# Performance work log

Measured on AMD Instinct MI355X. Metric: run time of the kernel, lower is better.

Reference implementation:

```python
import math
import jax, jax.numpy as jnp
import numpy as np
from jax import lax

L = 16
T = 256
FDIM = 3
N_MIN = 4
N_MAX = 64
INIT_RANGE = 1e-4
# low 32 bits of the products are exact in uint32, and XOR + (% T) with T=256
# only reads the low 8 bits, so uint32 arithmetic matches torch's int64 exactly.
PI = jnp.array([1, 2654435761, 805459861], dtype=jnp.uint32)

def _levels():
    growth = math.exp(math.log(N_MAX / N_MIN) / (L - 1))
    return [math.floor(N_MIN * growth ** l) for l in range(L)]

def setup_inputs() -> dict:
    key = jax.random.key(0)
    kx, kt = jax.random.split(key)
    x = jax.random.uniform(kx, (4, 3, 64, 64, 64), dtype=jnp.float32)
    hash_table = (jax.random.uniform(kt, (L, T, FDIM), dtype=jnp.float32) * 2.0
                  - 1.0) * INIT_RANGE
    return {"x": x, "hash_table": hash_table}

def _forward(x, hash_table):
    b, c, h, w, d = x.shape
    outs = []
    for l, n in enumerate(_levels()):
        kh, kw, kd = h // n, w // n, d // n
        # max_pool3d with kernel==stride, VALID padding (torch default)
        pooled = lax.reduce_window(x * n, -jnp.inf, lax.max,
                                   (1, 1, kh, kw, kd), (1, 1, kh, kw, kd),
                                   'VALID')  # [b, 3, nh, nw, nd]
        g = pooled.astype(jnp.uint32)  # trunc toward zero (values >= 0)
        g = g * PI.reshape(1, 3, 1, 1, 1)
        gh = (g[:, 0] ^ g[:, 1] ^ g[:, 2]) % jnp.uint32(T)  # [b, nh, nw, nd]
        feat = hash_table[l][gh]                 # [b, nh, nw, nd, F] gather
        feat = jnp.transpose(feat, (0, 4, 1, 3, 2))  # [b, F, nh, nd, nw]
        up = jax.image.resize(feat, (b, FDIM, h, w, d), method='trilinear')
        outs.append(up)
    return jnp.concatenate(outs, axis=1)  # [b, L*F, h, w, d]

def reference(x, hash_table):
    return _forward(x, hash_table)
```

## Files before the change

### kernel.cpp

```cpp
#include <hip/hip_runtime.h>
#include <cmath>
#include <cstdint>
#include <cstddef>

using u32 = unsigned int;
typedef float f32x4 __attribute__((ext_vector_type(4)));

__device__ inline void nt_store4(float* p, float a, float b, float c, float d)
{
    f32x4 v; v.x = a; v.y = b; v.z = c; v.w = d;
    __builtin_nontemporal_store(v, (f32x4*)p);
}

constexpr int NH[12] = {4,4,5,6,8,10,12,16,21,21,32,32};

constexpr int OFF_M2  = 0;
constexpr int OFF_M3  = 393216;
constexpr int OFF_M5  = 504348;
constexpr int OFF_M4  = 525084;
constexpr int OFF_M6  = 574236;
constexpr int OFF_M8  = 586236;
constexpr int OFF_M10 = 592380;
constexpr int OFF_M12 = 594972;
constexpr int OFF_M16 = 596472;

constexpr int GOFF[12] = {149310,149566,149822,150322,151186,153234,
                          157234,164146,180530,217574,254618,385690};

constexpr float invf_of(int nh){ return (float)(1.0/(64.0/(double)nh)); }
constexpr float INVF[12] = {invf_of(4),invf_of(4),invf_of(5),invf_of(6),
                            invf_of(8),invf_of(10),invf_of(12),invf_of(16),
                            invf_of(21),invf_of(21),invf_of(32),invf_of(32)};

struct HP { int n[16]; };

__device__ inline float lp(float a, float b, float w){ return fmaf(w, b - a, a); }

__device__ inline void hash_store(const float* __restrict__ tbl, float4* __restrict__ g4,
                                  int goff, int lvl, int n,
                                  float m0, float m1, float m2, int idx)
{
    float nf = (float)n;
    u32 g0 = (u32)(m0 * nf);
    u32 g1 = ((u32)(m1 * nf)) * 2654435761u;
    u32 g2 = ((u32)(m2 * nf)) * 805459861u;
    u32 h  = (g0 ^ g1 ^ g2) & 255u;
    const float* te = tbl + ((size_t)lvl * 256 + h) * 3;
    g4[goff + idx] = make_float4(te[0], te[1], te[2], 0.0f);
}

__global__ __launch_bounds__(256) void k_pool_base(const float* __restrict__ x,
                                                   float* __restrict__ ws)
{
    int tid = blockIdx.x * 256 + threadIdx.x;
    if (tid < 393216) {
        int pd = tid & 31, pw = (tid >> 5) & 31, ph = (tid >> 10) & 31;
        int bc = tid >> 15;
        const float* xp = x + (size_t)bc * 262144 + (ph*2)*4096 + (pw*2)*64 + pd*2;
        float2 v00 = *(const float2*)(xp);
        float2 v01 = *(const float2*)(xp + 64);
        float2 v10 = *(const float2*)(xp + 4096);
        float2 v11 = *(const float2*)(xp + 4160);
        float m = fmaxf(fmaxf(fmaxf(v00.x,v00.y), fmaxf(v01.x,v01.y)),
                        fmaxf(fmaxf(v10.x,v10.y), fmaxf(v11.x,v11.y)));
        ws[OFF_M2 + tid] = m;
    } else if (tid < 504348) {
        int idx = tid - 393216;
        int pd = idx % 21; int t2 = idx / 21;
        int pw = t2 % 21;  int t3 = t2 / 21;
        int ph = t3 % 21;  int bc = t3 / 21;
        const float* xp = x + (size_t)bc * 262144 + (ph*3)*4096 + (pw*3)*64 + pd*3;
        float m = -1.f;
        #pragma unroll
        for (int dh = 0; dh < 3; ++dh)
        #pragma unroll
        for (int dw = 0; dw < 3; ++dw) {
            const float* r = xp + dh*4096 + dw*64;
            m = fmaxf(m, fmaxf(fmaxf(r[0], r[1]), r[2]));
        }
        ws[OFF_M3 + idx] = m;
    } else if (tid < 525084) {
        int idx = tid - 504348;
        int pd = idx % 12; int t2 = idx / 12;
        int pw = t2 % 12;  int t3 = t2 / 12;
        int ph = t3 % 12;  int bc = t3 / 12;
        const float* xp = x + (size_t)bc * 262144 + (ph*5)*4096 + (pw*5)*64 + pd*5;
        float m = -1.f;
        #pragma unroll
        for (int dh = 0; dh < 5; ++dh)
        #pragma unroll
        for (int dw = 0; dw < 5; ++dw) {
            const float* r = xp + dh*4096 + dw*64;
            m = fmaxf(m, fmaxf(fmaxf(fmaxf(r[0],r[1]), fmaxf(r[2],r[3])), r[4]));
        }
        ws[OFF_M5 + idx] = m;
    }
}

__global__ __launch_bounds__(256) void k_pyr(const float* __restrict__ tbl,
                                             float* __restrict__ ws, HP hp)
{
    int tid = blockIdx.x * 256 + threadIdx.x;
    float4* g4 = (float4*)ws;
    if (tid < 49152) {
        int w = tid >> 6, lane = tid & 63;
        int pd = w & 3, pw = (w >> 2) & 3, ph = (w >> 4) & 3, bc = w >> 6;
        const float* m2 = ws + OFF_M2 + (size_t)bc*32768 + (ph*8)*1024 + (pw*8)*32 + pd*8;
        float m = -1.f;
        #pragma unroll
        for (int e = 0; e < 8; ++e) {
            int id2 = (e << 6) | lane;
            int dd = id2 & 7, dw = (id2 >> 3) & 7, dh = id2 >> 6;
            m = fmaxf(m, m2[dh*1024 + dw*32 + dd]);
        }
        #pragma unroll
        for (int s = 32; s; s >>= 1) m = fmaxf(m, __shfl_xor(m, s, 64));
        if (lane == 0) ws[OFF_M16 + w] = m;
    } else if (tid < 98304) {
        int idx = tid - 49152;
        int pd = idx & 15, pw = (idx >> 4) & 15, ph = (idx >> 8) & 15, bc = idx >> 12;
        const float* m2 = ws + OFF_M2 + (size_t)bc*32768 + (ph*2)*1024 + (pw*2)*32 + pd*2;
        float2 u0 = *(const float2*)(m2);
        float2 u1 = *(const float2*)(m2 + 32);
        float2 u2 = *(const float2*)(m2 + 1024);
        float2 u3 = *(const float2*)(m2 + 1056);
        ws[OFF_M4 + idx] = fmaxf(fmaxf(fmaxf(u0.x,u0.y), fmaxf(u1.x,u1.y)),
                                 fmaxf(fmaxf(u2.x,u2.y), fmaxf(u3.x,u3.y)));
    } else if (tid < 110304) {
        int idx = tid - 98304;
        int pd = idx % 10; int t2 = idx / 10;
        int pw = t2 % 10;  int t3 = t2 / 10;
        int ph = t3 % 10;  int bc = t3 / 10;
        const float* m2 = ws + OFF_M2 + (size_t)bc*32768 + (ph*3)*1024 + (pw*3)*32 + pd*3;
        float m = -1.f;
        #pragma unroll
        for (int dh = 0; dh < 3; ++dh)
        #pragma unroll
        for (int dw = 0; dw < 3; ++dw) {
            const float* r = m2 + dh*1024 + dw*32;
            m = fmaxf(m, fmaxf(fmaxf(r[0], r[1]), r[2]));
        }
        ws[OFF_M6 + idx] = m;
    } else if (tid < 116448) {
        int idx = tid - 110304;
        int pd = idx & 7, pw = (idx >> 3) & 7, ph = (idx >> 6) & 7, bc = idx >> 9;
        const float* m2 = ws + OFF_M2 + (size_t)bc*32768 + (ph*4)*1024 + (pw*4)*32 + pd*4;
        float m = -1.f;
        #pragma unroll
        for (int dh = 0; dh < 4; ++dh)
        #pragma unroll
        for (int dw = 0; dw < 4; ++dw) {
            float4 v = *(const float4*)(m2 + dh*1024 + dw*32);
            m = fmaxf(m, fmaxf(fmaxf(v.x,v.y), fmaxf(v.z,v.w)));
        }
        ws[OFF_M8 + idx] = m;
    } else if (tid < 119040) {
        int idx = tid - 116448;
        int pd = idx % 6; int t2 = idx / 6;
        int pw = t2 % 6;  int t3 = t2 / 6;
        int ph = t3 % 6;  int bc = t3 / 6;
        const float* m2 = ws + OFF_M2 + (size_t)bc*32768 + (ph*5)*1024 + (pw*5)*32 + pd*5;
        float m = -1.f;
        #pragma unroll
        for (int dh = 0; dh < 5; ++dh)
        #pragma unroll
        for (int dw = 0; dw < 5; ++dw) {
            const float* r = m2 + dh*1024 + dw*32;
            m = fmaxf(m, fmaxf(fmaxf(fmaxf(r[0],r[1]), fmaxf(r[2],r[3])), r[4]));
        }
        ws[OFF_M10 + idx] = m;
    } else if (tid < 120540) {
        int idx = tid - 119040;
        int pd = idx % 5; int t2 = idx / 5;
        int pw = t2 % 5;  int t3 = t2 / 5;
        int ph = t3 % 5;  int bc = t3 / 5;
        const float* m3 = ws + OFF_M3 + (size_t)bc*9261 + (ph*4)*441 + (pw*4)*21 + pd*4;
        float m = -1.f;
        #pragma unroll
        for (int dh = 0; dh < 4; ++dh)
        #pragma unroll
        for (int dw = 0; dw < 4; ++dw) {
            const float* r = m3 + dh*441 + dw*21;
            m = fmaxf(m, fmaxf(fmaxf(r[0],r[1]), fmaxf(r[2],r[3])));
        }
        ws[OFF_M12 + idx] = m;
    } else if (tid < 251612) {
        int idx = tid - 120540;
        int q = idx & 31, r = (idx >> 5) & 31, p = (idx >> 10) & 31, b = idx >> 15;
        int o = (p << 10) + (q << 5) + r;
        const float* M = ws + OFF_M2 + (size_t)b * 98304;
        float m0 = M[o], m1 = M[o + 32768], m2 = M[o + 65536];
        hash_store(tbl, g4, GOFF[10], 10, hp.n[10], m0, m1, m2, idx);
        hash_store(tbl, g4, GOFF[11], 11, hp.n[11], m0, m1, m2, idx);
    } else if (tid < 288656) {
        int idx = tid - 251612;
        int q = idx % 21; int t2 = idx / 21;
        int r = t2 % 21;  int t3 = t2 / 21;
        int p = t3 % 21;  int b = t3 / 21;
        int o = p*441 + q*21 + r;
        const float* M = ws + OFF_M3 + (size_t)b * 27783;
        float m0 = M[o], m1 = M[o + 9261], m2 = M[o + 18522];
        hash_store(tbl, g4, GOFF[8], 8, hp.n[8], m0, m1, m2, idx);
        hash_store(tbl, g4, GOFF[9], 9, hp.n[9], m0, m1, m2, idx);
    }
}

__global__ __launch_bounds__(256) void k_gather_small(const float* __restrict__ tbl,
                                                      float* __restrict__ ws, HP hp)
{
    int tid = blockIdx.x * 256 + threadIdx.x;
    float4* g4 = (float4*)ws;
    if (tid < 256) {
        int q = tid & 3, r = (tid >> 2) & 3, p = (tid >> 4) & 3, b = tid >> 6;
        const float* M = ws + OFF_M16 + (size_t)b * 192;
        int o = p*16 + q*4 + r;
        float m0 = M[o], m1 = M[o + 64], m2 = M[o + 128];
        hash_store(tbl, g4, GOFF[0], 0, hp.n[0], m0, m1, m2, tid);
        hash_store(tbl, g4, GOFF[1], 1, hp.n[1], m0, m1, m2, tid);
    } else if (tid < 756) {
        int idx = tid - 256;
        int q = idx % 5; int t2 = idx / 5;
        int r = t2 % 5;  int t3 = t2 / 5;
        int p = t3 % 5;  int b = t3 / 5;
        const float* M = ws + OFF_M12 + (size_t)b * 375;
        int o = p*25 + q*5 + r;
        hash_store(tbl, g4, GOFF[2], 2, hp.n[2], M[o], M[o+125], M[o+250], idx);
    } else if (tid < 1620) {
        int idx = tid - 756;
        int q = idx % 6; int t2 = idx / 6;
        int r = t2 % 6;  int t3 = t2 / 6;
        int p = t3 % 6;  int b = t3 / 6;
        const float* M = ws + OFF_M10 + (size_t)b * 648;
        int o = p*36 + q*6 + r;
        hash_store(tbl, g4, GOFF[3], 3, hp.n[3], M[o], M[o+216], M[o+432], idx);
    } else if (tid < 3668) {
        int idx = tid - 1620;
        int q = idx & 7, r = (idx >> 3) & 7, p = (idx >> 6) & 7, b = idx >> 9;
        const float* M = ws + OFF_M8 + (size_t)b * 1536;
        int o = p*64 + q*8 + r;
        hash_store(tbl, g4, GOFF[4], 4, hp.n[4], M[o], M[o+512], M[o+1024], idx);
    } else if (tid < 7668) {
        int idx = tid - 3668;
        int q = idx % 10; int t2 = idx / 10;
        int r = t2 % 10;  int t3 = t2 / 10;
        int p = t3 % 10;  int b = t3 / 10;
        const float* M = ws + OFF_M6 + (size_t)b * 3000;
        int o = p*100 + q*10 + r;
        hash_store(tbl, g4, GOFF[5], 5, hp.n[5], M[o], M[o+1000], M[o+2000], idx);
    } else if (tid < 14580) {
        int idx = tid - 7668;
        int q = idx % 12; int t2 = idx / 12;
        int r = t2 % 12;  int t3 = t2 / 12;
        int p = t3 % 12;  int b = t3 / 12;
        const float* M = ws + OFF_M5 + (size_t)b * 5184;
        int o = p*144 + q*12 + r;
        hash_store(tbl, g4, GOFF[6], 6, hp.n[6], M[o], M[o+1728], M[o+3456], idx);
    } else if (tid < 30964) {
        int idx = tid - 14580;
        int q = idx & 15, r = (idx >> 4) & 15, p = (idx >> 8) & 15, b = idx >> 12;
        const float* M = ws + OFF_M4 + (size_t)b * 12288;
        int o = p*256 + q*16 + r;
        hash_store(tbl, g4, GOFF[7], 7, hp.n[7], M[o], M[o+4096], M[o+8192], idx);
    }
}

__global__ __launch_bounds__(512) void k_identity(const float* __restrict__ x,
                                                  const float* __restrict__ tbl,
                                                  float* __restrict__ out, HP hp)
{
    __shared__ float  xs[3 * 4160];
    __shared__ float4 tab[1024];
    const int t = threadIdx.x;
    const int b = blockIdx.x >> 6, i = blockIdx.x & 63;

    for (int v = t; v < 1024; v += 512) {
        const float* te = tbl + (size_t)(3072 + v) * 3;
        tab[v] = make_float4(te[0], te[1], te[2], 0.f);
    }
    const float* xp = x + (size_t)b * 786432 + (size_t)i * 4096;
    #pragma unroll
    for (int c = 0; c < 3; ++c)
        for (int k = t; k < 4096; k += 512)
            xs[c * 4160 + (k >> 6) * 65 + (k & 63)] = xp[(size_t)c * 262144 + k];
    __syncthreads();

    float nfs[4] = {(float)hp.n[12], (float)hp.n[13],
                    (float)hp.n[14], (float)hp.n[15]};
    float* op = out + (size_t)b * 12582912 + (size_t)36 * 262144 + (size_t)i * 4096;

    #pragma unroll
    for (int it = 0; it < 2; ++it) {
        int pos = it * 512 + t;
        int j = pos >> 4, d0 = (pos & 15) << 2;
        float xv[3][4];
        #pragma unroll
        for (int dd = 0; dd < 4; ++dd) {
            int wrow = (d0 + dd) * 65 + j;
            xv[0][dd] = xs[wrow];
            xv[1][dd] = xs[4160 + wrow];
            xv[2][dd] = xs[8320 + wrow];
        }
        #pragma unroll
        for (int u = 0; u < 4; ++u) {
            float4 f[4];
            #pragma unroll
            for (int dd = 0; dd < 4; ++dd) {
                u32 g0 = (u32)(xv[0][dd] * nfs[u]);
                u32 g1 = ((u32)(xv[1][dd] * nfs[u])) * 2654435761u;
                u32 g2 = ((u32)(xv[2][dd] * nfs[u])) * 805459861u;
                f[dd] = tab[(u << 8) | ((g0 ^ g1 ^ g2) & 255u)];
            }
            int off = u * 786432 + j * 64 + d0;
            nt_store4(op + off,          f[0].x, f[1].x, f[2].x, f[3].x);
            nt_store4(op + off + 262144, f[0].y, f[1].y, f[2].y, f[3].y);
            nt_store4(op + off + 524288, f[0].z, f[1].z, f[2].z, f[3].z);
        }
    }
}

__global__ __launch_bounds__(256) void k_interp(const float* __restrict__ ws,
                                                float* __restrict__ out)
{
    __shared__ float4 plane[1024];
    const int t = threadIdx.x;
    const int l = blockIdx.y;
    const int b = blockIdx.x >> 6, i = blockIdx.x & 63;
    const int nh = NH[l];
    const float iv = INVF[l];
    const float4* g4 = (const float4*)ws;

    float fi = (float)i + 0.5f;
    float pp = fminf(fmaxf(fi * iv - 0.5f, 0.f), (float)(nh - 1));
    int p0 = min((int)pp, nh - 2);
    float wp = pp - (float)p0;
    const float4* Gp0 = g4 + GOFF[l] + (size_t)b * (nh * nh * nh) + p0 * nh * nh;
    const float4* Gp1 = Gp0 + nh * nh;
    for (int idx = t; idx < nh * nh; idx += 256) {
        float4 a = Gp0[idx], c = Gp1[idx];
        plane[idx] = make_float4(lp(a.x, c.x, wp), lp(a.y, c.y, wp),
                                 lp(a.z, c.z, wp), 0.f);
    }
    __syncthreads();

    float* op = out + (size_t)b * 12582912 + (size_t)(3 * l) * 262144 + (size_t)i * 4096;
    #pragma unroll
    for (int it = 0; it < 4; ++it) {
        int pos = it * 256 + t;
        int j = pos >> 4, d0 = (pos & 15) << 2;
        float fj = (float)j + 0.5f;
        float pr = fminf(fmaxf(fj * iv - 0.5f, 0.f), (float)(nh - 1));
        int r0 = min((int)pr, nh - 2);
        float wr = pr - (float)r0;
        const float4* P0 = plane + r0 * nh;
        const float4* P1 = P0 + nh;
        float ox[4], oy[4], oz[4];
        #pragma unroll
        for (int dd = 0; dd < 4; ++dd) {
            float fk = (float)(d0 + dd) + 0.5f;
            float pq = fminf(fmaxf(fk * iv - 0.5f, 0.f), (float)(nh - 1));
            int q0 = min((int)pq, nh - 2);
            float wq = pq - (float)q0;
            float4 A = P0[q0], B = P0[q0 + 1];
            float4 C = P1[q0], D = P1[q0 + 1];
            float tx = lp(A.x, B.x, wq), bx = lp(C.x, D.x, wq);
            float ty = lp(A.y, B.y, wq), by = lp(C.y, D.y, wq);
            float tz = lp(A.z, B.z, wq), bz = lp(C.z, D.z, wq);
            ox[dd] = lp(tx, bx, wr);
            oy[dd] = lp(ty, by, wr);
            oz[dd] = lp(tz, bz, wr);
        }
        int off = j * 64 + d0;
        nt_store4(op + off,          ox[0], ox[1], ox[2], ox[3]);
        nt_store4(op + off + 262144, oy[0], oy[1], oy[2], oy[3]);
        nt_store4(op + off + 524288, oz[0], oz[1], oz[2], oz[3]);
    }
}

extern "C" void kernel_launch(void* const* d_in, const int* in_sizes, int n_in,
                              void* d_out, int out_size, void* d_ws, size_t ws_size,
                              hipStream_t stream)
{
    const float* x   = (const float*)d_in[0];
    const float* tbl = (const float*)d_in[1];
    float* out = (float*)d_out;
    float* ws  = (float*)d_ws;

    HP hp;
    double growth = std::exp(std::log(16.0) / 15.0);
    for (int l = 0; l < 16; ++l)
        hp.n[l] = (int)std::floor(4.0 * std::pow(growth, (double)l));

    hipLaunchKernelGGL(k_pool_base,    dim3(2052),     dim3(256), 0, stream, x, ws);
    hipLaunchKernelGGL(k_pyr,          dim3(1128),     dim3(256), 0, stream, tbl, ws, hp);
    hipLaunchKernelGGL(k_gather_small, dim3(121),      dim3(256), 0, stream, tbl, ws, hp);
    hipLaunchKernelGGL(k_identity,     dim3(256),      dim3(512), 0, stream, x, tbl, out, hp);
    hipLaunchKernelGGL(k_interp,       dim3(256, 12),  dim3(256), 0, stream, ws, out);
}
```

Measured before the change: 65.72 us.

## Fuse hashing and table gather into interpolation kernel, split identity blocks

Hashing and table gather move out of the separate pyramid and small-gather passes and into k_interp, which now hashes the pooled maxima for its two planes on the fly and writes transposed plane entries with a padded pitch. This removes one kernel launch and the workspace round-trip of the gathered float4 features. k_identity now uses 256-thread blocks, each covering half a row, so it launches twice as many blocks with less shared memory each. In exchange, k_interp recomputes hashes per block (neighbouring i rows share planes) and does dependent table loads from global memory.

```diff
diff --git a/kernel.cpp b/kernel.cpp
--- a/kernel.cpp
+++ b/kernel.cpp
@@ -24,8 +24,8 @@
 constexpr int OFF_M12 = 594972;
 constexpr int OFF_M16 = 596472;
 
-constexpr int GOFF[12] = {149310,149566,149822,150322,151186,153234,
-                          157234,164146,180530,217574,254618,385690};
+constexpr int POFF[12] = {OFF_M16,OFF_M16,OFF_M12,OFF_M10,OFF_M8,OFF_M6,
+                          OFF_M5, OFF_M4, OFF_M3, OFF_M3, OFF_M2, OFF_M2};
 
 constexpr float invf_of(int nh){ return (float)(1.0/(64.0/(double)nh)); }
 constexpr float INVF[12] = {invf_of(4),invf_of(4),invf_of(5),invf_of(6),
@@ -35,19 +35,6 @@
 struct HP { int n[16]; };
 
 __device__ inline float lp(float a, float b, float w){ return fmaf(w, b - a, a); }
-
-__device__ inline void hash_store(const float* __restrict__ tbl, float4* __restrict__ g4,
-                                  int goff, int lvl, int n,
-                                  float m0, float m1, float m2, int idx)
-{
-    float nf = (float)n;
-    u32 g0 = (u32)(m0 * nf);
-    u32 g1 = ((u32)(m1 * nf)) * 2654435761u;
-    u32 g2 = ((u32)(m2 * nf)) * 805459861u;
-    u32 h  = (g0 ^ g1 ^ g2) & 255u;
-    const float* te = tbl + ((size_t)lvl * 256 + h) * 3;
-    g4[goff + idx] = make_float4(te[0], te[1], te[2], 0.0f);
-}
 
 __global__ __launch_bounds__(256) void k_pool_base(const float* __restrict__ x,
                                                    float* __restrict__ ws)
@@ -97,11 +84,9 @@
     }
 }
 
-__global__ __launch_bounds__(256) void k_pyr(const float* __restrict__ tbl,
-                                             float* __restrict__ ws, HP hp)
+__global__ __launch_bounds__(256) void k_pyr(float* __restrict__ ws)
 {
     int tid = blockIdx.x * 256 + threadIdx.x;
-    float4* g4 = (float4*)ws;
     if (tid < 49152) {
         int w = tid >> 6, lane = tid & 63;
         int pd = w & 3, pw = (w >> 2) & 3, ph = (w >> 4) & 3, bc = w >> 6;
@@ -184,121 +169,49 @@
             m = fmaxf(m, fmaxf(fmaxf(r[0],r[1]), fmaxf(r[2],r[3])));
         }
         ws[OFF_M12 + idx] = m;
-    } else if (tid < 251612) {
-        int idx = tid - 120540;
-        int q = idx & 31, r = (idx >> 5) & 31, p = (idx >> 10) & 31, b = idx >> 15;
-        int o = (p << 10) + (q << 5) + r;
-        const float* M = ws + OFF_M2 + (size_t)b * 98304;
-        float m0 = M[o], m1 = M[o + 32768], m2 = M[o + 65536];
-        hash_store(tbl, g4, GOFF[10], 10, hp.n[10], m0, m1, m2, idx);
-        hash_store(tbl, g4, GOFF[11], 11, hp.n[11], m0, m1, m2, idx);
-    } else if (tid < 288656) {
-        int idx = tid - 251612;
-        int q = idx % 21; int t2 = idx / 21;
-        int r = t2 % 21;  int t3 = t2 / 21;
-        int p = t3 % 21;  int b = t3 / 21;
-        int o = p*441 + q*21 + r;
-        const float* M = ws + OFF_M3 + (size_t)b * 27783;
-        float m0 = M[o], m1 = M[o + 9261], m2 = M[o + 18522];
-        hash_store(tbl, g4, GOFF[8], 8, hp.n[8], m0, m1, m2, idx);
-        hash_store(tbl, g4, GOFF[9], 9, hp.n[9], m0, m1, m2, idx);
-    }
-}
-
-__global__ __launch_bounds__(256) void k_gather_small(const float* __restrict__ tbl,
-                                                      float* __restrict__ ws, HP hp)
-{
-    int tid = blockIdx.x * 256 + threadIdx.x;
-    float4* g4 = (float4*)ws;
-    if (tid < 256) {
-        int q = tid & 3, r = (tid >> 2) & 3, p = (tid >> 4) & 3, b = tid >> 6;
-        const float* M = ws + OFF_M16 + (size_t)b * 192;
-        int o = p*16 + q*4 + r;
-        float m0 = M[o], m1 = M[o + 64], m2 = M[o + 128];
-        hash_store(tbl, g4, GOFF[0], 0, hp.n[0], m0, m1, m2, tid);
-        hash_store(tbl, g4, GOFF[1], 1, hp.n[1], m0, m1, m2, tid);
-    } else if (tid < 756) {
-        int idx = tid - 256;
-        int q = idx % 5; int t2 = idx / 5;
-        int r = t2 % 5;  int t3 = t2 / 5;
-        int p = t3 % 5;  int b = t3 / 5;
-        const float* M = ws + OFF_M12 + (size_t)b * 375;
-        int o = p*25 + q*5 + r;
-        hash_store(tbl, g4, GOFF[2], 2, hp.n[2], M[o], M[o+125], M[o+250], idx);
-    } else if (tid < 1620) {
-        int idx = tid - 756;
-        int q = idx % 6; int t2 = idx / 6;
-        int r = t2 % 6;  int t3 = t2 / 6;
-        int p = t3 % 6;  int b = t3 / 6;
-        const float* M = ws + OFF_M10 + (size_t)b * 648;
-        int o = p*36 + q*6 + r;
-        hash_store(tbl, g4, GOFF[3], 3, hp.n[3], M[o], M[o+216], M[o+432], idx);
-    } else if (tid < 3668) {
-        int idx = tid - 1620;
-        int q = idx & 7, r = (idx >> 3) & 7, p = (idx >> 6) & 7, b = idx >> 9;
-        const float* M = ws + OFF_M8 + (size_t)b * 1536;
-        int o = p*64 + q*8 + r;
-        hash_store(tbl, g4, GOFF[4], 4, hp.n[4], M[o], M[o+512], M[o+1024], idx);
-    } else if (tid < 7668) {
-        int idx = tid - 3668;
-        int q = idx % 10; int t2 = idx / 10;
-        int r = t2 % 10;  int t3 = t2 / 10;
-        int p = t3 % 10;  int b = t3 / 10;
-        const float* M = ws + OFF_M6 + (size_t)b * 3000;
-        int o = p*100 + q*10 + r;
-        hash_store(tbl, g4, GOFF[5], 5, hp.n[5], M[o], M[o+1000], M[o+2000], idx);
-    } else if (tid < 14580) {
-        int idx = tid - 7668;
-        int q = idx % 12; int t2 = idx / 12;
-        int r = t2 % 12;  int t3 = t2 / 12;
-        int p = t3 % 12;  int b = t3 / 12;
-        const float* M = ws + OFF_M5 + (size_t)b * 5184;
-        int o = p*144 + q*12 + r;
-        hash_store(tbl, g4, GOFF[6], 6, hp.n[6], M[o], M[o+1728], M[o+3456], idx);
-    } else if (tid < 30964) {
-        int idx = tid - 14580;
-        int q = idx & 15, r = (idx >> 4) & 15, p = (idx >> 8) & 15, b = idx >> 12;
-        const float* M = ws + OFF_M4 + (size_t)b * 12288;
-        int o = p*256 + q*16 + r;
-        hash_store(tbl, g4, GOFF[7], 7, hp.n[7], M[o], M[o+4096], M[o+8192], idx);
-    }
-}
-
-__global__ __launch_bounds__(512) void k_identity(const float* __restrict__ x,
+    }
+}
+
+__global__ __launch_bounds__(256) void k_identity(const float* __restrict__ x,
                                                   const float* __restrict__ tbl,
                                                   float* __restrict__ out, HP hp)
 {
-    __shared__ float  xs[3 * 4160];
+    __shared__ float  xs[3 * 2112];
     __shared__ float4 tab[1024];
     const int t = threadIdx.x;
-    const int b = blockIdx.x >> 6, i = blockIdx.x & 63;
-
-    for (int v = t; v < 1024; v += 512) {
+    const int b = blockIdx.x >> 7;
+    const int i = (blockIdx.x >> 1) & 63;
+    const int jh = blockIdx.x & 1;
+
+    for (int v = t; v < 1024; v += 256) {
         const float* te = tbl + (size_t)(3072 + v) * 3;
         tab[v] = make_float4(te[0], te[1], te[2], 0.f);
     }
-    const float* xp = x + (size_t)b * 786432 + (size_t)i * 4096;
+    const float* xp = x + (size_t)b * 786432 + (size_t)i * 4096 + jh * 32;
     #pragma unroll
     for (int c = 0; c < 3; ++c)
-        for (int k = t; k < 4096; k += 512)
-            xs[c * 4160 + (k >> 6) * 65 + (k & 63)] = xp[(size_t)c * 262144 + k];
+        for (int k = t; k < 2048; k += 256) {
+            int w = k >> 5, jl = k & 31;
+            xs[c * 2112 + w * 33 + jl] = xp[(size_t)c * 262144 + w * 64 + jl];
+        }
     __syncthreads();
 
     float nfs[4] = {(float)hp.n[12], (float)hp.n[13],
                     (float)hp.n[14], (float)hp.n[15]};
-    float* op = out + (size_t)b * 12582912 + (size_t)36 * 262144 + (size_t)i * 4096;
+    float* op = out + (size_t)b * 12582912 + (size_t)36 * 262144
+                    + (size_t)i * 4096 + jh * 2048;
 
     #pragma unroll
     for (int it = 0; it < 2; ++it) {
-        int pos = it * 512 + t;
-        int j = pos >> 4, d0 = (pos & 15) << 2;
+        int pos = it * 256 + t;
+        int jl = pos >> 4, d0 = (pos & 15) << 2;
         float xv[3][4];
         #pragma unroll
         for (int dd = 0; dd < 4; ++dd) {
-            int wrow = (d0 + dd) * 65 + j;
+            int wrow = (d0 + dd) * 33 + jl;
             xv[0][dd] = xs[wrow];
-            xv[1][dd] = xs[4160 + wrow];
-            xv[2][dd] = xs[8320 + wrow];
+            xv[1][dd] = xs[2112 + wrow];
+            xv[2][dd] = xs[4224 + wrow];
         }
         #pragma unroll
         for (int u = 0; u < 4; ++u) {
@@ -310,7 +223,7 @@
                 u32 g2 = ((u32)(xv[2][dd] * nfs[u])) * 805459861u;
                 f[dd] = tab[(u << 8) | ((g0 ^ g1 ^ g2) & 255u)];
             }
-            int off = u * 786432 + j * 64 + d0;
+            int off = u * 786432 + jl * 64 + d0;
             nt_store4(op + off,          f[0].x, f[1].x, f[2].x, f[3].x);
             nt_store4(op + off + 262144, f[0].y, f[1].y, f[2].y, f[3].y);
             nt_store4(op + off + 524288, f[0].z, f[1].z, f[2].z, f[3].z);
@@ -319,26 +232,42 @@
 }
 
 __global__ __launch_bounds__(256) void k_interp(const float* __restrict__ ws,
-                                                float* __restrict__ out)
-{
-    __shared__ float4 plane[1024];
+                                                const float* __restrict__ tbl,
+                                                float* __restrict__ out, HP hp)
+{
+    __shared__ float4 plane[1056];
     const int t = threadIdx.x;
     const int l = blockIdx.y;
     const int b = blockIdx.x >> 6, i = blockIdx.x & 63;
     const int nh = NH[l];
+    const int pitch = nh + 1;
     const float iv = INVF[l];
-    const float4* g4 = (const float4*)ws;
+    const float nf = (float)hp.n[l];
 
     float fi = (float)i + 0.5f;
     float pp = fminf(fmaxf(fi * iv - 0.5f, 0.f), (float)(nh - 1));
     int p0 = min((int)pp, nh - 2);
     float wp = pp - (float)p0;
-    const float4* Gp0 = g4 + GOFF[l] + (size_t)b * (nh * nh * nh) + p0 * nh * nh;
-    const float4* Gp1 = Gp0 + nh * nh;
-    for (int idx = t; idx < nh * nh; idx += 256) {
-        float4 a = Gp0[idx], c = Gp1[idx];
-        plane[idx] = make_float4(lp(a.x, c.x, wp), lp(a.y, c.y, wp),
-                                 lp(a.z, c.z, wp), 0.f);
+
+    const int nsq = nh * nh, ncb = nsq * nh;
+    const float* M   = ws + POFF[l] + (size_t)b * 3 * ncb;
+    const float* Mp0 = M + p0 * nsq;
+    const float* Mp1 = Mp0 + nsq;
+    const float* tl  = tbl + (size_t)l * 768;
+
+    for (int idx = t; idx < nsq; idx += 256) {
+        int w = idx / nh, d = idx - w * nh;
+        float a0 = Mp0[idx], a1 = Mp0[idx + ncb], a2 = Mp0[idx + 2*ncb];
+        u32 h0 = ((u32)(a0*nf) ^ (((u32)(a1*nf))*2654435761u)
+                               ^ (((u32)(a2*nf))*805459861u)) & 255u;
+        const float* t0 = tl + h0 * 3;
+        float b0 = Mp1[idx], b1 = Mp1[idx + ncb], b2 = Mp1[idx + 2*ncb];
+        u32 h1 = ((u32)(b0*nf) ^ (((u32)(b1*nf))*2654435761u)
+                               ^ (((u32)(b2*nf))*805459861u)) & 255u;
+        const float* t1 = tl + h1 * 3;
+        plane[d * pitch + w] = make_float4(lp(t0[0], t1[0], wp),
+                                           lp(t0[1], t1[1], wp),
+                                           lp(t0[2], t1[2], wp), 0.f);
     }
     __syncthreads();
 
@@ -351,8 +280,8 @@
         float pr = fminf(fmaxf(fj * iv - 0.5f, 0.f), (float)(nh - 1));
         int r0 = min((int)pr, nh - 2);
         float wr = pr - (float)r0;
-        const float4* P0 = plane + r0 * nh;
-        const float4* P1 = P0 + nh;
+        const float4* P0 = plane + r0 * pitch;
+        const float4* P1 = P0 + pitch;
         float ox[4], oy[4], oz[4];
         #pragma unroll
         for (int dd = 0; dd < 4; ++dd) {
@@ -390,9 +319,8 @@
     for (int l = 0; l < 16; ++l)
         hp.n[l] = (int)std::floor(4.0 * std::pow(growth, (double)l));
 
-    hipLaunchKernelGGL(k_pool_base,    dim3(2052),     dim3(256), 0, stream, x, ws);
-    hipLaunchKernelGGL(k_pyr,          dim3(1128),     dim3(256), 0, stream, tbl, ws, hp);
-    hipLaunchKernelGGL(k_gather_small, dim3(121),      dim3(256), 0, stream, tbl, ws, hp);
-    hipLaunchKernelGGL(k_identity,     dim3(256),      dim3(512), 0, stream, x, tbl, out, hp);
-    hipLaunchKernelGGL(k_interp,       dim3(256, 12),  dim3(256), 0, stream, ws, out);
-}
+    hipLaunchKernelGGL(k_pool_base, dim3(2052),    dim3(256), 0, stream, x, ws);
+    hipLaunchKernelGGL(k_pyr,       dim3(471),     dim3(256), 0, stream, ws);
+    hipLaunchKernelGGL(k_identity,  dim3(512),     dim3(256), 0, stream, x, tbl, out, hp);
+    hipLaunchKernelGGL(k_interp,    dim3(256, 12), dim3(256), 0, stream, ws, tbl, out, hp);
+}
```

Result: faster. 61.33 us (-6.7%).
